# Kernel tuning notes

Measured on AMD Instinct MI355X. Metric: run time of the kernel, lower is better.

The kernel has to match this reference:

```python
import jax, jax.numpy as jnp
import numpy as np

DIM = 192
WIN = 7
HEADS = 6
N = WIN * WIN
B_ = 8192
NW = 1024  # windows per image; B_ // NW images


def _relative_position_index(win):
    coords = np.stack(np.meshgrid(np.arange(win), np.arange(win), indexing='ij'))  # [2,Wh,Ww]
    flat = coords.reshape(2, -1)  # [2,N]
    rel = flat[:, :, None] - flat[:, None, :]  # [2,N,N]
    rel = rel.transpose(1, 2, 0)
    rel[..., 0] += win - 1
    rel[..., 1] += win - 1
    rel[..., 0] *= 2 * win - 1
    return jnp.asarray(rel[..., 0] + rel[..., 1], dtype=jnp.int32)  # [N,N]


def setup_inputs() -> dict:
    key = jax.random.key(0)
    ks = jax.random.split(key, 7)
    x = jax.random.normal(ks[0], (B_, WIN, WIN, DIM), dtype=jnp.float32)
    mask = jnp.zeros((NW, N, N), dtype=jnp.float32)
    qkv_w = jax.random.normal(ks[1], (3 * DIM, DIM), dtype=jnp.float32) * 0.02
    qkv_b = jnp.zeros((3 * DIM,), dtype=jnp.float32)
    proj_w = jax.random.normal(ks[2], (DIM, DIM), dtype=jnp.float32) * 0.02
    proj_b = jnp.zeros((DIM,), dtype=jnp.float32)
    num_rel = (2 * WIN - 1) * (2 * WIN - 1)
    rel_bias_table = jax.random.truncated_normal(ks[3], -2.0, 2.0, (num_rel, HEADS), dtype=jnp.float32) * 0.02
    rel_index = _relative_position_index(WIN)
    return {"x": x, "mask": mask, "qkv_w": qkv_w, "qkv_b": qkv_b,
            "proj_w": proj_w, "proj_b": proj_b,
            "rel_bias_table": rel_bias_table, "rel_index": rel_index}


def reference(x, mask, qkv_w, qkv_b, proj_w, proj_b, rel_bias_table, rel_index):
    Bw, Wh, Ww, C = x.shape
    n = Wh * Ww
    H = HEADS
    hd = C // H
    scale = hd ** -0.5
    xf = x.reshape(Bw, n, C)
    qkv = xf @ qkv_w.T + qkv_b  # [Bw, n, 3C]
    qkv = qkv.reshape(Bw, n, 3, H, hd).transpose(2, 0, 3, 1, 4)  # [3, Bw, H, n, hd]
    q, k, v = qkv[0], qkv[1], qkv[2]
    attn = jnp.einsum('bhnd,bhmd->bhnm', q * scale, k)  # [Bw, H, n, n]
    bias = rel_bias_table[rel_index.reshape(-1)].reshape(n, n, H).transpose(2, 0, 1)  # [H,n,n]
    attn = attn + bias[None]
    nw = mask.shape[0]
    attn = attn.reshape(Bw // nw, nw, H, n, n) + mask[None, :, None]
    attn = attn.reshape(Bw, H, n, n)
    attn = jax.nn.softmax(attn, axis=-1)
    out = jnp.einsum('bhnm,bhmd->bhnd', attn, v)  # [Bw,H,n,hd]
    out = out.transpose(0, 2, 1, 3).reshape(Bw, n, C)
    return out @ proj_w.T + proj_b
```

## Files before the change

kernel.cpp:

```cpp
#include <hip/hip_runtime.h>
#include <hip/hip_bf16.h>

#define NSEQ 49
#define DIMC 192
#define NHEAD 6
#define NWIN 1024
#define NBLK 8192
#define NN 2401
#define QSCALE 0.17677669529663687f

typedef __bf16 bf16x8 __attribute__((ext_vector_type(8)));
typedef float f32x4 __attribute__((ext_vector_type(4)));
typedef unsigned int u32x4 __attribute__((ext_vector_type(4)));
typedef unsigned short u16;

#define WQ_OFF 0
#define WP_OFF 221184
#define BIAS_OFF 294912
#define QB_OFF 352544
#define PB_OFF 354848

__device__ __forceinline__ u16 f2bf(float f) {
  unsigned int u = __builtin_bit_cast(unsigned int, f);
  u += 0x7fffu + ((u >> 16) & 1u);
  return (u16)(u >> 16);
}
__device__ __forceinline__ f32x4 mfma16(bf16x8 a, bf16x8 b, f32x4 c) {
  return __builtin_amdgcn_mfma_f32_16x16x32_bf16(a, b, c, 0, 0, 0);
}
__device__ __forceinline__ f32x4 ld4u(const float* p) {
  f32x4 v; __builtin_memcpy(&v, p, 16); return v;
}
__device__ __forceinline__ bf16x8 pack8(f32x4 a, f32x4 b) {
  u32x4 w;
  w[0] = f2bf(a[0]) | ((unsigned)f2bf(a[1]) << 16);
  w[1] = f2bf(a[2]) | ((unsigned)f2bf(a[3]) << 16);
  w[2] = f2bf(b[0]) | ((unsigned)f2bf(b[1]) << 16);
  w[3] = f2bf(b[2]) | ((unsigned)f2bf(b[3]) << 16);
  return __builtin_bit_cast(bf16x8, w);
}

__global__ void prep_kernel(const float* __restrict__ qkv_w, const float* __restrict__ qkv_b,
                            const float* __restrict__ proj_w, const float* __restrict__ proj_b,
                            const float* __restrict__ table, const int* __restrict__ ridx,
                            char* __restrict__ ws) {
  u16* wq = (u16*)(ws + WQ_OFF);
  u16* wp = (u16*)(ws + WP_OFF);
  float* biasf = (float*)(ws + BIAS_OFF);
  float* qb = (float*)(ws + QB_OFF);
  float* pb = (float*)(ws + PB_OFF);
  int idx = blockIdx.x * blockDim.x + threadIdx.x;
  const int T0 = 576*192, T1 = T0 + 192*192, T2 = T1 + NHEAD*NN, T3 = T2 + 576, T4 = T3 + 192;
  if (idx < T0) {
    float f = qkv_w[idx];
    if (idx < 192*192) f *= QSCALE;
    wq[idx] = f2bf(f);
  } else if (idx < T1) {
    int i = idx - T0;
    wp[i] = f2bf(proj_w[i]);
  } else if (idx < T2) {
    int i = idx - T1;
    int h = i / NN, rc = i - h*NN;
    biasf[i] = table[ridx[rc]*NHEAD + h];
  } else if (idx < T3) {
    int i = idx - T2;
    qb[i] = qkv_b[i] * (i < 192 ? QSCALE : 1.0f);
  } else if (idx < T4) {
    int i = idx - T3;
    pb[i] = proj_b[i];
  }
}

__global__ __launch_bounds__(384, 2)
void wattn_kernel(const float* __restrict__ x, const float* __restrict__ mask,
                  const char* __restrict__ ws, float* __restrict__ out) {
  __shared__ __align__(16) char smem[73728];
  char* qkb = smem;
  char* vsb = smem + 49152;

  const u16* wq = (const u16*)(ws + WQ_OFF);
  const u16* wp = (const u16*)(ws + WP_OFF);
  const float* biasf = (const float*)(ws + BIAS_OFF);
  const float* qb = (const float*)(ws + QB_OFF);
  const float* pb = (const float*)(ws + PB_OFF);

  const int tid = threadIdx.x;
  const int wave = tid >> 6;
  const int lane = tid & 63;
  const int lhi = lane >> 4, llo = lane & 15;
  const int win = blockIdx.x;
  const int h = wave;

  bf16x8 xa[4][6];
  {
    const float* xp = x + (size_t)win * (NSEQ*DIMC);
    #pragma unroll
    for (int rt = 0; rt < 4; ++rt) {
      int row = rt*16 + llo;
      bool valid = (row < NSEQ);
      const float* pr = xp + row*DIMC + lhi*8;
      #pragma unroll
      for (int kk = 0; kk < 6; ++kk) {
        f32x4 f0 = {0.f,0.f,0.f,0.f}, f1 = {0.f,0.f,0.f,0.f};
        if (valid) { f0 = *(const f32x4*)(pr + kk*32); f1 = *(const f32x4*)(pr + kk*32 + 4); }
        xa[rt][kk] = pack8(f0, f1);
      }
    }
  }

  #pragma unroll
  for (int cc = 0; cc < 6; ++cc) {
    int s = (cc < 2) ? (wave*2 + cc)
          : (cc < 4) ? (12 + wave*2 + (cc - 2))
                     : (24 + wave*2 + (cc - 4));
    const u16* wrow = wq + (s*16 + llo)*DIMC + lhi*8;
    bf16x8 b0 = *(const bf16x8*)(wrow +   0);
    bf16x8 b1 = *(const bf16x8*)(wrow +  32);
    bf16x8 b2 = *(const bf16x8*)(wrow +  64);
    bf16x8 b3 = *(const bf16x8*)(wrow +  96);
    bf16x8 b4 = *(const bf16x8*)(wrow + 128);
    bf16x8 b5 = *(const bf16x8*)(wrow + 160);
    float bn = qb[s*16 + llo];
    #pragma unroll
    for (int rt = 0; rt < 4; ++rt) {
      f32x4 acc = {0.f,0.f,0.f,0.f};
      acc = mfma16(xa[rt][0], b0, acc);
      acc = mfma16(xa[rt][1], b1, acc);
      acc = mfma16(xa[rt][2], b2, acc);
      acc = mfma16(xa[rt][3], b3, acc);
      acc = mfma16(xa[rt][4], b4, acc);
      acc = mfma16(xa[rt][5], b5, acc);
      if (cc < 4) {
        int col = s*16 + llo;
        #pragma unroll
        for (int i = 0; i < 4; ++i) {
          int row = rt*16 + lhi*4 + i;
          *(u16*)(qkb + row*768 + ((col*2) ^ ((row&7)<<4))) = f2bf(acc[i] + bn);
        }
      } else {
        int d = (s - 24)*16 + llo;
        #pragma unroll
        for (int i = 0; i < 4; ++i) {
          int seq = rt*16 + lhi*4 + i;
          *(u16*)(vsb + d*128 + ((seq*2) ^ ((d&7)<<4))) = f2bf(acc[i] + bn);
        }
      }
    }
  }

  __syncthreads();

  bf16x8 kf[4], qf[4];
  #pragma unroll
  for (int tt = 0; tt < 4; ++tt) {
    int row = tt*16 + llo;
    kf[tt] = *(const bf16x8*)(qkb + row*768 + ((((192 + h*32)*2) + lhi*16) ^ ((row&7)<<4)));
    qf[tt] = *(const bf16x8*)(qkb + row*768 + ((((h*32)*2) + lhi*16) ^ ((row&7)<<4)));
  }
  f32x4 t[4][4];
  #pragma unroll
  for (int kt = 0; kt < 4; ++kt)
    #pragma unroll
    for (int qt = 0; qt < 4; ++qt) {
      f32x4 z = {0.f,0.f,0.f,0.f};
      t[kt][qt] = mfma16(kf[kt], qf[qt], z);
    }

  {
    const float* brow = biasf + h*NN;
    const float* mrow = mask + (size_t)(win & (NWIN-1))*NN;
    #pragma unroll
    for (int qt = 0; qt < 4; ++qt) {
      int q = qt*16 + llo;
      if (q < NSEQ) {
        #pragma unroll
        for (int kt = 0; kt < 3; ++kt) {
          int kb = kt*16 + lhi*4;
          f32x4 b4 = ld4u(brow + q*NSEQ + kb);
          f32x4 m4 = ld4u(mrow + q*NSEQ + kb);
          #pragma unroll
          for (int i = 0; i < 4; ++i) t[kt][qt][i] += b4[i] + m4[i];
        }
        if (lhi == 0) t[3][qt][0] += brow[q*NSEQ + 48] + mrow[q*NSEQ + 48];
      }
    }
  }

  unsigned int pk[4][4][2];
  #pragma unroll
  for (int qt = 0; qt < 4; ++qt) {
    float m = -1e30f;
    #pragma unroll
    for (int kt = 0; kt < 3; ++kt)
      #pragma unroll
      for (int i = 0; i < 4; ++i) m = fmaxf(m, t[kt][qt][i]);
    if (lhi == 0) m = fmaxf(m, t[3][qt][0]);
    m = fmaxf(m, __shfl_xor(m, 16));
    m = fmaxf(m, __shfl_xor(m, 32));
    float sum = 0.f;
    #pragma unroll
    for (int kt = 0; kt < 3; ++kt)
      #pragma unroll
      for (int i = 0; i < 4; ++i) { float e = __expf(t[kt][qt][i] - m); t[kt][qt][i] = e; sum += e; }
    { float e = (lhi == 0) ? __expf(t[3][qt][0] - m) : 0.f; t[3][qt][0] = e; sum += e; }
    t[3][qt][1] = 0.f; t[3][qt][2] = 0.f; t[3][qt][3] = 0.f;
    sum += __shfl_xor(sum, 16);
    sum += __shfl_xor(sum, 32);
    float inv = 1.f / sum;
    #pragma unroll
    for (int kt = 0; kt < 4; ++kt) {
      float p0 = t[kt][qt][0]*inv, p1 = t[kt][qt][1]*inv;
      float p2 = t[kt][qt][2]*inv, p3 = t[kt][qt][3]*inv;
      pk[kt][qt][0] = f2bf(p0) | ((unsigned)f2bf(p1) << 16);
      pk[kt][qt][1] = f2bf(p2) | ((unsigned)f2bf(p3) << 16);
    }
  }

  f32x4 o[4][2];
  #pragma unroll
  for (int qt = 0; qt < 4; ++qt)
    #pragma unroll
    for (int dt = 0; dt < 2; ++dt) o[qt][dt] = (f32x4){0.f,0.f,0.f,0.f};
  #pragma unroll
  for (int kk = 0; kk < 2; ++kk) {
    bf16x8 pa[4];
    #pragma unroll
    for (int qt = 0; qt < 4; ++qt) {
      u32x4 w;
      #pragma unroll
      for (int ee = 0; ee < 4; ++ee) {
        int src = (((lhi & 1)*2 + (ee >> 1)) << 4) + llo;
        int wA = __shfl((int)pk[2*kk    ][qt][ee & 1], src);
        int wB = __shfl((int)pk[2*kk + 1][qt][ee & 1], src);
        w[ee] = (lhi < 2) ? (unsigned)wA : (unsigned)wB;
      }
      pa[qt] = __builtin_bit_cast(bf16x8, w);
    }
    #pragma unroll
    for (int dt = 0; dt < 2; ++dt) {
      int dg = h*32 + dt*16 + llo;
      bf16x8 vf = *(const bf16x8*)(vsb + dg*128 + ((kk*64 + lhi*16) ^ ((dg&7)<<4)));
      #pragma unroll
      for (int qt = 0; qt < 4; ++qt) o[qt][dt] = mfma16(pa[qt], vf, o[qt][dt]);
    }
  }

  #pragma unroll
  for (int qt = 0; qt < 4; ++qt)
    #pragma unroll
    for (int dt = 0; dt < 2; ++dt)
      #pragma unroll
      for (int i = 0; i < 4; ++i) {
        int row = qt*16 + lhi*4 + i;
        int col = h*32 + dt*16 + llo;
        *(u16*)(qkb + row*768 + ((col*2) ^ ((row&7)<<4))) = f2bf(o[qt][dt][i]);
      }

  __syncthreads();

  #pragma unroll
  for (int ss = 0; ss < 2; ++ss) {
    int s = wave + ss*6;
    const u16* wrow = wp + (s*16 + llo)*DIMC + lhi*8;
    bf16x8 b0 = *(const bf16x8*)(wrow +   0);
    bf16x8 b1 = *(const bf16x8*)(wrow +  32);
    bf16x8 b2 = *(const bf16x8*)(wrow +  64);
    bf16x8 b3 = *(const bf16x8*)(wrow +  96);
    bf16x8 b4 = *(const bf16x8*)(wrow + 128);
    bf16x8 b5 = *(const bf16x8*)(wrow + 160);
    float bn = pb[s*16 + llo];
    #pragma unroll
    for (int rt = 0; rt < 4; ++rt) {
      int arow = rt*16 + llo;
      f32x4 acc = {0.f,0.f,0.f,0.f};
      acc = mfma16(*(const bf16x8*)(qkb + arow*768 + ((  0 + lhi*16) ^ ((arow&7)<<4))), b0, acc);
      acc = mfma16(*(const bf16x8*)(qkb + arow*768 + (( 64 + lhi*16) ^ ((arow&7)<<4))), b1, acc);
      acc = mfma16(*(const bf16x8*)(qkb + arow*768 + ((128 + lhi*16) ^ ((arow&7)<<4))), b2, acc);
      acc = mfma16(*(const bf16x8*)(qkb + arow*768 + ((192 + lhi*16) ^ ((arow&7)<<4))), b3, acc);
      acc = mfma16(*(const bf16x8*)(qkb + arow*768 + ((256 + lhi*16) ^ ((arow&7)<<4))), b4, acc);
      acc = mfma16(*(const bf16x8*)(qkb + arow*768 + ((320 + lhi*16) ^ ((arow&7)<<4))), b5, acc);
      #pragma unroll
      for (int i = 0; i < 4; ++i) {
        int row = rt*16 + lhi*4 + i;
        if (row < NSEQ)
          out[((size_t)win*NSEQ + row)*DIMC + s*16 + llo] = acc[i] + bn;
      }
    }
  }
}

extern "C" void kernel_launch(void* const* d_in, const int* in_sizes, int n_in,
                              void* d_out, int out_size, void* d_ws, size_t ws_size,
                              hipStream_t stream) {
  const float* x      = (const float*)d_in[0];
  const float* mask   = (const float*)d_in[1];
  const float* qkv_w  = (const float*)d_in[2];
  const float* qkv_b  = (const float*)d_in[3];
  const float* proj_w = (const float*)d_in[4];
  const float* proj_b = (const float*)d_in[5];
  const float* table  = (const float*)d_in[6];
  const int*   ridx   = (const int*)d_in[7];
  float* out = (float*)d_out;
  char* ws = (char*)d_ws;

  const int prep_total = 576*192 + 192*192 + NHEAD*NN + 576 + 192;
  prep_kernel<<<(prep_total + 255)/256, 256, 0, stream>>>(qkv_w, qkv_b, proj_w, proj_b, table, ridx, ws);
  wattn_kernel<<<NBLK, 384, 0, stream>>>(x, mask, ws, out);
}
```

Before: 1.103 ms.

## Shrink LDS footprint and register pressure to raise occupancy in window attention

Removes the separate V shared buffer: V results are held in registers, then written into the now-free K-region of the QK buffer after Q/K fragments are loaded, with added barriers. The QKV projection is split into two row halves to cut live x registers, and the QK^T/softmax are fused per query tile instead of holding all scores. Launch bounds are raised from 2 to 5 blocks per CU, and manual bf16 rounding is replaced with native __bf16 conversions. Extra __syncthreads and tighter register budget may cause spills or stalls.

```diff
diff --git a/kernel.cpp b/kernel.cpp
--- a/kernel.cpp
+++ b/kernel.cpp
@@ -31,12 +31,19 @@
 __device__ __forceinline__ f32x4 ld4u(const float* p) {
   f32x4 v; __builtin_memcpy(&v, p, 16); return v;
 }
-__device__ __forceinline__ bf16x8 pack8(f32x4 a, f32x4 b) {
+__device__ __forceinline__ unsigned pkbf2(float lo, float hi) {
+  __bf16 a = (__bf16)lo, b = (__bf16)hi;
+  return (unsigned)__builtin_bit_cast(u16, a) | ((unsigned)__builtin_bit_cast(u16, b) << 16);
+}
+__device__ __forceinline__ void st_bf(char* p, float f) {
+  *(__bf16*)p = (__bf16)f;
+}
+__device__ __forceinline__ bf16x8 pack8f(f32x4 a, f32x4 b) {
   u32x4 w;
-  w[0] = f2bf(a[0]) | ((unsigned)f2bf(a[1]) << 16);
-  w[1] = f2bf(a[2]) | ((unsigned)f2bf(a[3]) << 16);
-  w[2] = f2bf(b[0]) | ((unsigned)f2bf(b[1]) << 16);
-  w[3] = f2bf(b[2]) | ((unsigned)f2bf(b[3]) << 16);
+  w[0] = pkbf2(a[0], a[1]);
+  w[1] = pkbf2(a[2], a[3]);
+  w[2] = pkbf2(b[0], b[1]);
+  w[3] = pkbf2(b[2], b[3]);
   return __builtin_bit_cast(bf16x8, w);
 }
 
@@ -71,12 +78,10 @@
   }
 }
 
-__global__ __launch_bounds__(384, 2)
+__global__ __launch_bounds__(384, 5)
 void wattn_kernel(const float* __restrict__ x, const float* __restrict__ mask,
                   const char* __restrict__ ws, float* __restrict__ out) {
-  __shared__ __align__(16) char smem[73728];
-  char* qkb = smem;
-  char* vsb = smem + 49152;
+  __shared__ __align__(16) char qkb[49152];
 
   const u16* wq = (const u16*)(ws + WQ_OFF);
   const u16* wp = (const u16*)(ws + WP_OFF);
@@ -91,58 +96,59 @@
   const int win = blockIdx.x;
   const int h = wave;
 
-  bf16x8 xa[4][6];
-  {
-    const float* xp = x + (size_t)win * (NSEQ*DIMC);
-    #pragma unroll
-    for (int rt = 0; rt < 4; ++rt) {
-      int row = rt*16 + llo;
-      bool valid = (row < NSEQ);
-      const float* pr = xp + row*DIMC + lhi*8;
-      #pragma unroll
-      for (int kk = 0; kk < 6; ++kk) {
-        f32x4 f0 = {0.f,0.f,0.f,0.f}, f1 = {0.f,0.f,0.f,0.f};
-        if (valid) { f0 = *(const f32x4*)(pr + kk*32); f1 = *(const f32x4*)(pr + kk*32 + 4); }
-        xa[rt][kk] = pack8(f0, f1);
-      }
-    }
-  }
-
-  #pragma unroll
-  for (int cc = 0; cc < 6; ++cc) {
-    int s = (cc < 2) ? (wave*2 + cc)
-          : (cc < 4) ? (12 + wave*2 + (cc - 2))
-                     : (24 + wave*2 + (cc - 4));
-    const u16* wrow = wq + (s*16 + llo)*DIMC + lhi*8;
-    bf16x8 b0 = *(const bf16x8*)(wrow +   0);
-    bf16x8 b1 = *(const bf16x8*)(wrow +  32);
-    bf16x8 b2 = *(const bf16x8*)(wrow +  64);
-    bf16x8 b3 = *(const bf16x8*)(wrow +  96);
-    bf16x8 b4 = *(const bf16x8*)(wrow + 128);
-    bf16x8 b5 = *(const bf16x8*)(wrow + 160);
-    float bn = qb[s*16 + llo];
-    #pragma unroll
-    for (int rt = 0; rt < 4; ++rt) {
-      f32x4 acc = {0.f,0.f,0.f,0.f};
-      acc = mfma16(xa[rt][0], b0, acc);
-      acc = mfma16(xa[rt][1], b1, acc);
-      acc = mfma16(xa[rt][2], b2, acc);
-      acc = mfma16(xa[rt][3], b3, acc);
-      acc = mfma16(xa[rt][4], b4, acc);
-      acc = mfma16(xa[rt][5], b5, acc);
-      if (cc < 4) {
-        int col = s*16 + llo;
+  unsigned vp[2][2][2][2];
+  #pragma unroll
+  for (int half = 0; half < 2; ++half) {
+    bf16x8 xa[2][6];
+    {
+      const float* xp = x + (size_t)win * (NSEQ*DIMC);
+      #pragma unroll
+      for (int r2 = 0; r2 < 2; ++r2) {
+        int row = (half*2 + r2)*16 + llo;
+        bool valid = (row < NSEQ);
+        const float* pr = xp + row*DIMC + lhi*8;
         #pragma unroll
-        for (int i = 0; i < 4; ++i) {
-          int row = rt*16 + lhi*4 + i;
-          *(u16*)(qkb + row*768 + ((col*2) ^ ((row&7)<<4))) = f2bf(acc[i] + bn);
+        for (int kk = 0; kk < 6; ++kk) {
+          f32x4 f0 = {0.f,0.f,0.f,0.f}, f1 = {0.f,0.f,0.f,0.f};
+          if (valid) { f0 = *(const f32x4*)(pr + kk*32); f1 = *(const f32x4*)(pr + kk*32 + 4); }
+          xa[r2][kk] = pack8f(f0, f1);
         }
-      } else {
-        int d = (s - 24)*16 + llo;
-        #pragma unroll
-        for (int i = 0; i < 4; ++i) {
-          int seq = rt*16 + lhi*4 + i;
-          *(u16*)(vsb + d*128 + ((seq*2) ^ ((d&7)<<4))) = f2bf(acc[i] + bn);
+      }
+    }
+    #pragma unroll
+    for (int cc = 0; cc < 6; ++cc) {
+      int s = (cc < 2) ? (h*2 + cc)
+            : (cc < 4) ? (12 + h*2 + (cc - 2))
+                       : (24 + h*2 + (cc - 4));
+      const u16* wrow = wq + (s*16 + llo)*DIMC + lhi*8;
+      bf16x8 b0 = *(const bf16x8*)(wrow +   0);
+      bf16x8 b1 = *(const bf16x8*)(wrow +  32);
+      bf16x8 b2 = *(const bf16x8*)(wrow +  64);
+      bf16x8 b3 = *(const bf16x8*)(wrow +  96);
+      bf16x8 b4 = *(const bf16x8*)(wrow + 128);
+      bf16x8 b5 = *(const bf16x8*)(wrow + 160);
+      float bn = qb[s*16 + llo];
+      #pragma unroll
+      for (int r2 = 0; r2 < 2; ++r2) {
+        f32x4 acc = {0.f,0.f,0.f,0.f};
+        acc = mfma16(xa[r2][0], b0, acc);
+        acc = mfma16(xa[r2][1], b1, acc);
+        acc = mfma16(xa[r2][2], b2, acc);
+        acc = mfma16(xa[r2][3], b3, acc);
+        acc = mfma16(xa[r2][4], b4, acc);
+        acc = mfma16(xa[r2][5], b5, acc);
+        int rt = half*2 + r2;
+        if (cc < 4) {
+          int col = s*16 + llo;
+          #pragma unroll
+          for (int i = 0; i < 4; ++i) {
+            int row = rt*16 + lhi*4 + i;
+            st_bf(qkb + row*768 + ((col*2) ^ ((row&7)<<4)), acc[i] + bn);
+          }
+        } else {
+          int c = cc - 4;
+          vp[half][c][r2][0] = pkbf2(acc[0] + bn, acc[1] + bn);
+          vp[half][c][r2][1] = pkbf2(acc[2] + bn, acc[3] + bn);
         }
       }
     }
@@ -157,20 +163,36 @@
     kf[tt] = *(const bf16x8*)(qkb + row*768 + ((((192 + h*32)*2) + lhi*16) ^ ((row&7)<<4)));
     qf[tt] = *(const bf16x8*)(qkb + row*768 + ((((h*32)*2) + lhi*16) ^ ((row&7)<<4)));
   }
-  f32x4 t[4][4];
-  #pragma unroll
-  for (int kt = 0; kt < 4; ++kt)
-    #pragma unroll
-    for (int qt = 0; qt < 4; ++qt) {
-      f32x4 z = {0.f,0.f,0.f,0.f};
-      t[kt][qt] = mfma16(kf[kt], qf[qt], z);
-    }
-
+
+  __syncthreads();
+
+  #pragma unroll
+  for (int c = 0; c < 2; ++c) {
+    int d = (2*h + c)*16 + llo;
+    char* vb = qkb + (d&63)*768 + 384 + (d>>6)*128;
+    int sw = (d&7)<<4;
+    #pragma unroll
+    for (int half = 0; half < 2; ++half)
+      #pragma unroll
+      for (int r2 = 0; r2 < 2; ++r2) {
+        int seq0 = (half*2 + r2)*16 + lhi*4;
+        *(unsigned*)(vb + ((seq0*2)     ^ sw)) = vp[half][c][r2][0];
+        *(unsigned*)(vb + ((seq0*2 + 4) ^ sw)) = vp[half][c][r2][1];
+      }
+  }
+
+  unsigned pk[4][4][2];
   {
     const float* brow = biasf + h*NN;
     const float* mrow = mask + (size_t)(win & (NWIN-1))*NN;
     #pragma unroll
     for (int qt = 0; qt < 4; ++qt) {
+      f32x4 tq[4];
+      #pragma unroll
+      for (int kt = 0; kt < 4; ++kt) {
+        f32x4 z = {0.f,0.f,0.f,0.f};
+        tq[kt] = mfma16(kf[kt], qf[qt], z);
+      }
       int q = qt*16 + llo;
       if (q < NSEQ) {
         #pragma unroll
@@ -179,42 +201,37 @@
           f32x4 b4 = ld4u(brow + q*NSEQ + kb);
           f32x4 m4 = ld4u(mrow + q*NSEQ + kb);
           #pragma unroll
-          for (int i = 0; i < 4; ++i) t[kt][qt][i] += b4[i] + m4[i];
+          for (int i = 0; i < 4; ++i) tq[kt][i] += b4[i] + m4[i];
         }
-        if (lhi == 0) t[3][qt][0] += brow[q*NSEQ + 48] + mrow[q*NSEQ + 48];
-      }
-    }
-  }
-
-  unsigned int pk[4][4][2];
-  #pragma unroll
-  for (int qt = 0; qt < 4; ++qt) {
-    float m = -1e30f;
-    #pragma unroll
-    for (int kt = 0; kt < 3; ++kt)
-      #pragma unroll
-      for (int i = 0; i < 4; ++i) m = fmaxf(m, t[kt][qt][i]);
-    if (lhi == 0) m = fmaxf(m, t[3][qt][0]);
-    m = fmaxf(m, __shfl_xor(m, 16));
-    m = fmaxf(m, __shfl_xor(m, 32));
-    float sum = 0.f;
-    #pragma unroll
-    for (int kt = 0; kt < 3; ++kt)
-      #pragma unroll
-      for (int i = 0; i < 4; ++i) { float e = __expf(t[kt][qt][i] - m); t[kt][qt][i] = e; sum += e; }
-    { float e = (lhi == 0) ? __expf(t[3][qt][0] - m) : 0.f; t[3][qt][0] = e; sum += e; }
-    t[3][qt][1] = 0.f; t[3][qt][2] = 0.f; t[3][qt][3] = 0.f;
-    sum += __shfl_xor(sum, 16);
-    sum += __shfl_xor(sum, 32);
-    float inv = 1.f / sum;
-    #pragma unroll
-    for (int kt = 0; kt < 4; ++kt) {
-      float p0 = t[kt][qt][0]*inv, p1 = t[kt][qt][1]*inv;
-      float p2 = t[kt][qt][2]*inv, p3 = t[kt][qt][3]*inv;
-      pk[kt][qt][0] = f2bf(p0) | ((unsigned)f2bf(p1) << 16);
-      pk[kt][qt][1] = f2bf(p2) | ((unsigned)f2bf(p3) << 16);
-    }
-  }
+        if (lhi == 0) tq[3][0] += brow[q*NSEQ + 48] + mrow[q*NSEQ + 48];
+      }
+      float m = -1e30f;
+      #pragma unroll
+      for (int kt = 0; kt < 3; ++kt)
+        #pragma unroll
+        for (int i = 0; i < 4; ++i) m = fmaxf(m, tq[kt][i]);
+      if (lhi == 0) m = fmaxf(m, tq[3][0]);
+      m = fmaxf(m, __shfl_xor(m, 16));
+      m = fmaxf(m, __shfl_xor(m, 32));
+      float sum = 0.f;
+      #pragma unroll
+      for (int kt = 0; kt < 3; ++kt)
+        #pragma unroll
+        for (int i = 0; i < 4; ++i) { float e = __expf(tq[kt][i] - m); tq[kt][i] = e; sum += e; }
+      { float e = (lhi == 0) ? __expf(tq[3][0] - m) : 0.f; tq[3][0] = e; sum += e; }
+      tq[3][1] = 0.f; tq[3][2] = 0.f; tq[3][3] = 0.f;
+      sum += __shfl_xor(sum, 16);
+      sum += __shfl_xor(sum, 32);
+      float inv = 1.f / sum;
+      #pragma unroll
+      for (int kt = 0; kt < 4; ++kt) {
+        pk[kt][qt][0] = pkbf2(tq[kt][0]*inv, tq[kt][1]*inv);
+        pk[kt][qt][1] = pkbf2(tq[kt][2]*inv, tq[kt][3]*inv);
+      }
+    }
+  }
+
+  __syncthreads();
 
   f32x4 o[4][2];
   #pragma unroll
@@ -239,7 +256,8 @@
     #pragma unroll
     for (int dt = 0; dt < 2; ++dt) {
       int dg = h*32 + dt*16 + llo;
-      bf16x8 vf = *(const bf16x8*)(vsb + dg*128 + ((kk*64 + lhi*16) ^ ((dg&7)<<4)));
+      bf16x8 vf = *(const bf16x8*)(qkb + (dg&63)*768 + 384 + ((dg>>6)*128)
+                                   + ((kk*64 + lhi*16) ^ ((dg&7)<<4)));
       #pragma unroll
       for (int qt = 0; qt < 4; ++qt) o[qt][dt] = mfma16(pa[qt], vf, o[qt][dt]);
     }
@@ -253,7 +271,7 @@
       for (int i = 0; i < 4; ++i) {
         int row = qt*16 + lhi*4 + i;
         int col = h*32 + dt*16 + llo;
-        *(u16*)(qkb + row*768 + ((col*2) ^ ((row&7)<<4))) = f2bf(o[qt][dt][i]);
+        st_bf(qkb + row*768 + ((col*2) ^ ((row&7)<<4)), o[qt][dt][i]);
       }
 
   __syncthreads();
```

Measured after the change: 1.966 ms. +78.2%, slower.
